# Performance work log

Measured on AMD Instinct MI355X. Metric: run time of the kernel, lower is better.

Reference implementation:

```python
import jax, jax.numpy as jnp
import numpy as np

COMMITMENT_COST = 0.25
DIST_SCALE = 400.0


def setup_inputs() -> dict:
    key = jax.random.key(0)
    ks = jax.random.split(key, 6)
    B, T, D, K = 64, 1024, 512, 512
    s = 1.0 / np.sqrt(D)
    return {
        "inputs": jax.random.normal(ks[0], (B, T, D), dtype=jnp.float32),
        "mean_W": jax.random.normal(ks[1], (D, D), dtype=jnp.float32) * s,
        "mean_b": jax.random.normal(ks[2], (D,), dtype=jnp.float32) * s,
        "logvar_W": jax.random.normal(ks[3], (D, K), dtype=jnp.float32) * s,
        "logvar_b": jax.random.normal(ks[4], (K,), dtype=jnp.float32) * s,
        "embedding": jax.random.normal(ks[5], (K, D), dtype=jnp.float32),
    }


def reference(inputs, mean_W, mean_b, logvar_W, logvar_b, embedding):
    sg = jax.lax.stop_gradient
    D = embedding.shape[1]
    flat = inputs.reshape(-1, D)                      # [N, D]
    x = flat @ mean_W + mean_b                        # mean_layer, [N, D]
    z_logvar = x @ logvar_W + logvar_b                # logvar_layer, [N, K]
    # squared euclidean distances to codebook, [N, K]
    distances = (
        jnp.sum(x * x, axis=1, keepdims=True)
        + jnp.sum(embedding * embedding, axis=1)
        - 2.0 * (x @ embedding.T)
    )
    smooth = jnp.exp(-2.0 * z_logvar)                 # 1/exp(logvar)^2
    d = distances / DIST_SCALE
    prob = jnp.exp(-d * (0.5 * smooth)) / jnp.sqrt(smooth)
    probs = prob / jnp.sum(prob, axis=1, keepdims=True)  # per-row normalize, [N, K]
    quantized = (probs @ embedding).reshape(inputs.shape)
    e_latent_loss = jnp.mean((sg(quantized) - inputs) ** 2)
    q_latent_loss = jnp.mean((quantized - sg(inputs)) ** 2)
    loss = q_latent_loss + COMMITMENT_COST * e_latent_loss
    quantized_st = inputs + sg(quantized - inputs)    # straight-through
    avg_probs = jnp.mean(probs, axis=0)
    perplexity = jnp.exp(-jnp.sum(avg_probs * jnp.log(avg_probs + 1e-10)))
    return loss, quantized_st, perplexity, probs
```

## Files before the change

kernel.cpp:

```cpp
#include <hip/hip_runtime.h>
#include <stdint.h>

#define BM 128
#define BN 128
#define BK 32
#define DIMD 512
#define NROWS 65536
#define QOFF 1
#define PERPOFF 33554433
#define PROBSOFF 33554434
#define NELEM 33554432

typedef __attribute__((ext_vector_type(8))) short bf16x8;
typedef __attribute__((ext_vector_type(4))) short s16x4;
typedef __attribute__((ext_vector_type(4))) float f32x4;

typedef const __attribute__((address_space(1))) void* gas_ptr;
typedef __attribute__((address_space(3))) void* las_ptr;

__device__ __forceinline__ short f2bf(float x){
  uint32_t u = __builtin_bit_cast(uint32_t, x);
  uint32_t r = (u + 0x7fffu + ((u >> 16) & 1u)) >> 16;
  return (short)(uint16_t)r;
}
__device__ __forceinline__ float bf2f(short h){
  return __builtin_bit_cast(float, ((uint32_t)(uint16_t)h) << 16);
}

__device__ __forceinline__ void stage_bf16(const short* __restrict__ g, int row0, int ld, int k0,
                                           short* lds){
  int tid = threadIdx.x;
#pragma unroll
  for (int i = 0; i < 2; ++i){
    int t = tid + i * 256;
    int row = t >> 2, c = t & 3;
    const short* src = g + (long)(row0 + row) * ld + k0 + c * 8;
    __builtin_amdgcn_global_load_lds((gas_ptr)src, (las_ptr)(lds + t * 8), 16, 0, 0);
  }
}

__device__ __forceinline__ void stage_f32_split(const float* __restrict__ g, int row0, int ld, int k0,
                                                short* hi, short* lo){
  int tid = threadIdx.x;
#pragma unroll
  for (int i = 0; i < 4; ++i){
    int t = tid + i * 256;
    int row = t >> 3, c = t & 7;
    const float4 v = *(const float4*)(g + (long)(row0 + row) * ld + k0 + c * 4);
    short h0 = f2bf(v.x), h1 = f2bf(v.y), h2 = f2bf(v.z), h3 = f2bf(v.w);
    s16x4 hv; hv[0] = h0; hv[1] = h1; hv[2] = h2; hv[3] = h3;
    s16x4 lv;
    lv[0] = f2bf(v.x - bf2f(h0)); lv[1] = f2bf(v.y - bf2f(h1));
    lv[2] = f2bf(v.z - bf2f(h2)); lv[3] = f2bf(v.w - bf2f(h3));
    *(s16x4*)(hi + row * BK + c * 4) = hv;
    *(s16x4*)(lo + row * BK + c * 4) = lv;
  }
}

__device__ __forceinline__ bf16x8 frag(const short* lds, int r, int q){
  return *(const bf16x8*)(lds + r * BK + q * 8);
}

__device__ __forceinline__ int swz4(int row, int c){ return c ^ ((row >> 1) & 3); }

__device__ __forceinline__ bf16x8 frag_s(const short* lds, int r, int q){
  return *(const bf16x8*)(lds + r * BK + swz4(r, q) * 8);
}

__device__ __forceinline__ void stage_B512(const short* __restrict__ g, int k0, short* lds){
  int tid = threadIdx.x;
#pragma unroll
  for (int i = 0; i < 4; ++i){
    int t = tid + i * 512;
    int row = t >> 2, c = t & 3;
    int cs = swz4(row, c);
    __builtin_amdgcn_global_load_lds((gas_ptr)(g + (long)row * DIMD + k0 + cs * 8),
                                     (las_ptr)(lds + t * 8), 16, 0, 0);
  }
}

__device__ __forceinline__ void stage_A64(const short* __restrict__ gh, const short* __restrict__ gl,
                                          int n0, int k0, short* Ah, short* Al){
  int tid = threadIdx.x;
  int t = tid & 255;
  int row = t >> 2, c = t & 3;
  int cs = swz4(row, c);
  const short* g = (tid < 256) ? gh : gl;
  short* lds = (tid < 256) ? Ah : Al;
  __builtin_amdgcn_global_load_lds((gas_ptr)(g + (long)(n0 + row) * DIMD + k0 + cs * 8),
                                   (las_ptr)(lds + t * 8), 16, 0, 0);
}

__device__ __forceinline__ void stage_A64h(const short* __restrict__ g, int n0, int k0, short* Ah){
  int tid = threadIdx.x;
  if (tid < 256){
    int row = tid >> 2, c = tid & 3;
    int cs = swz4(row, c);
    __builtin_amdgcn_global_load_lds((gas_ptr)(g + (long)(n0 + row) * DIMD + k0 + cs * 8),
                                     (las_ptr)(Ah + tid * 8), 16, 0, 0);
  }
}

__global__ __launch_bounds__(256) void k_convert_w(
    const float* __restrict__ meanW, const float* __restrict__ lvW, const float* __restrict__ emb,
    short* __restrict__ MWThi, short* __restrict__ MWTlo,
    short* __restrict__ VWThi, short* __restrict__ VWTlo,
    short* __restrict__ E, short* __restrict__ ET, float* __restrict__ enorm)
{
  int b = blockIdx.x;
  int tid = threadIdx.x;
  float esum = 0.f;
  for (int j = tid; j < 512; j += 256){
    float w = meanW[b * 512 + j];
    short h = f2bf(w); short l = f2bf(w - bf2f(h));
    MWThi[j * 512 + b] = h; MWTlo[j * 512 + b] = l;
    float v = lvW[b * 512 + j];
    h = f2bf(v); l = f2bf(v - bf2f(h));
    VWThi[j * 512 + b] = h; VWTlo[j * 512 + b] = l;
    float e = emb[b * 512 + j];
    short eh = f2bf(e);
    E[b * 512 + j] = eh;
    ET[j * 512 + b] = eh;
    esum += e * e;
  }
  for (int o = 32; o >= 1; o >>= 1) esum += __shfl_xor(esum, o);
  __shared__ float red[4];
  if ((tid & 63) == 0) red[tid >> 6] = esum;
  __syncthreads();
  if (tid == 0) enorm[b] = red[0] + red[1] + red[2] + red[3];
}

__global__ __launch_bounds__(256, 2) void k_gemm_mean(
    const float* __restrict__ inp, const short* __restrict__ Bhi, const short* __restrict__ Blo,
    const float* __restrict__ bias, short* __restrict__ Xhi, short* __restrict__ Xlo,
    float* __restrict__ xnorm)
{
  __shared__ short Ah[BM * BK], Al[BM * BK], Bh[BN * BK], Bl[BN * BK];
  int tid = threadIdx.x;
  int n0 = blockIdx.x * BM, c0 = blockIdx.y * BN;
  int lane = tid & 63, wid = tid >> 6;
  int wm = wid >> 1, wn = wid & 1;
  int q = lane >> 4, m = lane & 15;
  f32x4 acc[4][4];
#pragma unroll
  for (int i = 0; i < 4; i++)
#pragma unroll
    for (int j = 0; j < 4; j++)
#pragma unroll
      for (int r = 0; r < 4; r++) acc[i][j][r] = 0.f;

  for (int k0 = 0; k0 < DIMD; k0 += BK){
    __syncthreads();
    stage_f32_split(inp, n0, DIMD, k0, Ah, Al);
    stage_bf16(Bhi, c0, DIMD, k0, Bh);
    stage_bf16(Blo, c0, DIMD, k0, Bl);
    __syncthreads();
    bf16x8 ah[4], al[4], bh[4], bl[4];
#pragma unroll
    for (int i = 0; i < 4; i++){
      ah[i] = frag(Ah, wm * 64 + i * 16 + m, q);
      al[i] = frag(Al, wm * 64 + i * 16 + m, q);
      bh[i] = frag(Bh, wn * 64 + i * 16 + m, q);
      bl[i] = frag(Bl, wn * 64 + i * 16 + m, q);
    }
#pragma unroll
    for (int i = 0; i < 4; i++)
#pragma unroll
      for (int j = 0; j < 4; j++){
        acc[i][j] = __builtin_amdgcn_mfma_f32_16x16x32_bf16(ah[i], bh[j], acc[i][j], 0, 0, 0);
        acc[i][j] = __builtin_amdgcn_mfma_f32_16x16x32_bf16(ah[i], bl[j], acc[i][j], 0, 0, 0);
        acc[i][j] = __builtin_amdgcn_mfma_f32_16x16x32_bf16(al[i], bh[j], acc[i][j], 0, 0, 0);
      }
  }
#pragma unroll
  for (int i = 0; i < 4; i++){
#pragma unroll
    for (int r = 0; r < 4; r++){
      int row = n0 + wm * 64 + i * 16 + q * 4 + r;
      float xn = 0.f;
#pragma unroll
      for (int j = 0; j < 4; j++){
        int col = c0 + wn * 64 + j * 16 + m;
        float x = acc[i][j][r] + bias[col];
        short h = f2bf(x);
        short l = f2bf(x - bf2f(h));
        Xhi[(long)row * DIMD + col] = h;
        Xlo[(long)row * DIMD + col] = l;
        xn += x * x;
      }
      xn += __shfl_xor(xn, 1); xn += __shfl_xor(xn, 2);
      xn += __shfl_xor(xn, 4); xn += __shfl_xor(xn, 8);
      if (m == 0) atomicAdd(&xnorm[row], xn);
    }
  }
}

__global__ __launch_bounds__(512, 2) void k_fused(
    const short* __restrict__ Xh, const short* __restrict__ Xl,
    const short* __restrict__ Vh, const short* __restrict__ Vl,
    const short* __restrict__ Eb, const short* __restrict__ Et,
    const float* __restrict__ lvb, const float* __restrict__ xnorm,
    const float* __restrict__ enorm, const float* __restrict__ inp,
    float* __restrict__ probs, float* __restrict__ qout,
    float* __restrict__ Pacc, float* __restrict__ lossacc)
{
  __shared__ __align__(128) char pool[110592];
  short* Ah  = (short*)pool;
  short* Al  = (short*)(pool + 4096);
  short* Bv0 = (short*)(pool + 8192);
  short* Bv1 = (short*)(pool + 40960);
  short* Be  = (short*)(pool + 73728);
  float* rrA = (float*)(pool + 106496);
  float* rrB = (float*)(pool + 108544);
  short* P   = (short*)(pool + 8192);

  const int tid = threadIdx.x;
  const int n0 = blockIdx.x * 64;
  const int lane = tid & 63, wid = tid >> 6;
  const int q = lane >> 4, m = lane & 15;
  const int c0 = wid * 64;

  f32x4 accZ[4][4];
  f32x4 accS[4][4];
#pragma unroll
  for (int i = 0; i < 4; i++)
#pragma unroll
    for (int j = 0; j < 4; j++)
#pragma unroll
      for (int r = 0; r < 4; r++) accZ[i][j][r] = 0.f;

  stage_A64(Xh, Xl, n0, 0, Ah, Al);
  stage_B512(Vh, 0, Bv0);
  stage_B512(Vl, 0, Bv1);
  for (int k0 = 0; k0 < 512; k0 += 32){
    __syncthreads();
    bf16x8 ah[4], al[4], bh[4], bl[4];
#pragma unroll
    for (int i = 0; i < 4; i++){
      ah[i] = frag_s(Ah, i * 16 + m, q);
      al[i] = frag_s(Al, i * 16 + m, q);
    }
#pragma unroll
    for (int j = 0; j < 4; j++){
      bh[j] = frag_s(Bv0, c0 + j * 16 + m, q);
      bl[j] = frag_s(Bv1, c0 + j * 16 + m, q);
    }
    __syncthreads();
    if (k0 < 480){
      stage_A64(Xh, Xl, n0, k0 + 32, Ah, Al);
      stage_B512(Vh, k0 + 32, Bv0);
      stage_B512(Vl, k0 + 32, Bv1);
    }
#pragma unroll
    for (int j = 0; j < 4; j++)
#pragma unroll
      for (int i = 0; i < 4; i++){
        accZ[i][j] = __builtin_amdgcn_mfma_f32_16x16x32_bf16(ah[i], bh[j], accZ[i][j], 0, 0, 0);
        accZ[i][j] = __builtin_amdgcn_mfma_f32_16x16x32_bf16(ah[i], bl[j], accZ[i][j], 0, 0, 0);
        accZ[i][j] = __builtin_amdgcn_mfma_f32_16x16x32_bf16(al[i], bh[j], accZ[i][j], 0, 0, 0);
      }
  }

#pragma unroll
  for (int i = 0; i < 4; i++)
#pragma unroll
    for (int j = 0; j < 4; j++)
#pragma unroll
      for (int r = 0; r < 4; r++) accS[i][j][r] = 0.f;
  stage_A64h(Xh, n0, 0, Ah);
  stage_B512(Eb, 0, Be);
  for (int k0 = 0; k0 < 512; k0 += 32){
    __syncthreads();
    bf16x8 ah[4], be[4];
#pragma unroll
    for (int i = 0; i < 4; i++) ah[i] = frag_s(Ah, i * 16 + m, q);
#pragma unroll
    for (int j = 0; j < 4; j++) be[j] = frag_s(Be, c0 + j * 16 + m, q);
    __syncthreads();
    if (k0 < 480){
      stage_A64h(Xh, n0, k0 + 32, Ah);
      stage_B512(Eb, k0 + 32, Be);
    }
#pragma unroll
    for (int j = 0; j < 4; j++)
#pragma unroll
      for (int i = 0; i < 4; i++)
        accS[i][j] = __builtin_amdgcn_mfma_f32_16x16x32_bf16(ah[i], be[j], accS[i][j], 0, 0, 0);
  }

  float lvbv[4], env[4];
#pragma unroll
  for (int j = 0; j < 4; j++){
    int col = c0 + j * 16 + m;
    lvbv[j] = lvb[col];
    env[j] = enorm[col];
  }
  float xnv[4][4];
#pragma unroll
  for (int i = 0; i < 4; i++)
#pragma unroll
    for (int r = 0; r < 4; r++) xnv[i][r] = xnorm[n0 + i * 16 + q * 4 + r];

  const float inv800 = 0.5f / 400.0f;
#pragma unroll
  for (int i = 0; i < 4; i++)
#pragma unroll
    for (int j = 0; j < 4; j++)
#pragma unroll
      for (int r = 0; r < 4; r++){
        float z = accZ[i][j][r] + lvbv[j];
        float s = accS[i][j][r];
        float sm = __expf(-2.f * z);
        accS[i][j][r] = z - inv800 * (xnv[i][r] + env[j] - 2.f * s) * sm;
      }

  float mxp[4][4];
#pragma unroll
  for (int i = 0; i < 4; i++)
#pragma unroll
    for (int r = 0; r < 4; r++){
      float v = accS[i][0][r];
#pragma unroll
      for (int j = 1; j < 4; j++) v = fmaxf(v, accS[i][j][r]);
      v = fmaxf(v, __shfl_xor(v, 1));
      v = fmaxf(v, __shfl_xor(v, 2));
      v = fmaxf(v, __shfl_xor(v, 4));
      v = fmaxf(v, __shfl_xor(v, 8));
      mxp[i][r] = v;
    }
  if (m == 0){
#pragma unroll
    for (int i = 0; i < 4; i++)
#pragma unroll
      for (int r = 0; r < 4; r++)
        rrA[(i * 16 + q * 4 + r) * 8 + wid] = mxp[i][r];
  }
  __syncthreads();
  float mxf[4][4];
#pragma unroll
  for (int i = 0; i < 4; i++)
#pragma unroll
    for (int r = 0; r < 4; r++){
      int row = i * 16 + q * 4 + r;
      float v = rrA[row * 8 + 0];
#pragma unroll
      for (int w = 1; w < 8; w++) v = fmaxf(v, rrA[row * 8 + w]);
      mxf[i][r] = v;
    }

  float smr[4][4];
#pragma unroll
  for (int i = 0; i < 4; i++)
#pragma unroll
    for (int r = 0; r < 4; r++){
      float sacc = 0.f;
#pragma unroll
      for (int j = 0; j < 4; j++){
        float p = __expf(accS[i][j][r] - mxf[i][r]);
        accS[i][j][r] = p;
        sacc += p;
      }
      sacc += __shfl_xor(sacc, 1);
      sacc += __shfl_xor(sacc, 2);
      sacc += __shfl_xor(sacc, 4);
      sacc += __shfl_xor(sacc, 8);
      smr[i][r] = sacc;
    }
  if (m == 0){
#pragma unroll
    for (int i = 0; i < 4; i++)
#pragma unroll
      for (int r = 0; r < 4; r++)
        rrB[(i * 16 + q * 4 + r) * 8 + wid] = smr[i][r];
  }
  __syncthreads();
#pragma unroll
  for (int i = 0; i < 4; i++)
#pragma unroll
    for (int r = 0; r < 4; r++){
      int row = i * 16 + q * 4 + r;
      float v = 0.f;
#pragma unroll
      for (int w = 0; w < 8; w++) v += rrB[row * 8 + w];
      smr[i][r] = v;
    }

  float pj[4];
#pragma unroll
  for (int j = 0; j < 4; j++) pj[j] = 0.f;
#pragma unroll
  for (int i = 0; i < 4; i++)
#pragma unroll
    for (int r = 0; r < 4; r++){
      int rowl = i * 16 + q * 4 + r;
      long rowg = n0 + rowl;
      float inv = 1.0f / smr[i][r];
#pragma unroll
      for (int j = 0; j < 4; j++){
        int col = c0 + j * 16 + m;
        float qv = accS[i][j][r] * inv;
        probs[rowg * 512 + col] = qv;
        pj[j] += qv;
        int cg = col >> 3;
        P[rowl * 512 + ((((cg ^ (rowl & 7)) << 3)) | (col & 7))] = f2bf(qv);
      }
    }
#pragma unroll
  for (int j = 0; j < 4; j++){
    pj[j] += __shfl_xor(pj[j], 16);
    pj[j] += __shfl_xor(pj[j], 32);
  }
  if (lane < 16){
#pragma unroll
    for (int j = 0; j < 4; j++) atomicAdd(&Pacc[c0 + j * 16 + m], pj[j]);
  }

#pragma unroll
  for (int i = 0; i < 4; i++)
#pragma unroll
    for (int j = 0; j < 4; j++)
#pragma unroll
      for (int r = 0; r < 4; r++) accZ[i][j][r] = 0.f;
  stage_B512(Et, 0, Be);
  for (int k0 = 0; k0 < 512; k0 += 32){
    __syncthreads();
    bf16x8 pa[4], bq[4];
#pragma unroll
    for (int i = 0; i < 4; i++){
      int rowl = i * 16 + m;
      int cg = (k0 >> 3) + q;
      pa[i] = *(const bf16x8*)(P + rowl * 512 + ((cg ^ (rowl & 7)) << 3));
    }
#pragma unroll
    for (int j = 0; j < 4; j++) bq[j] = frag_s(Be, c0 + j * 16 + m, q);
    __syncthreads();
    if (k0 < 480) stage_B512(Et, k0 + 32, Be);
#pragma unroll
    for (int j = 0; j < 4; j++)
#pragma unroll
      for (int i = 0; i < 4; i++)
        accZ[i][j] = __builtin_amdgcn_mfma_f32_16x16x32_bf16(pa[i], bq[j], accZ[i][j], 0, 0, 0);
  }

  float lsum = 0.f;
#pragma unroll
  for (int i = 0; i < 4; i++)
#pragma unroll
    for (int r = 0; r < 4; r++){
      long rowg = n0 + i * 16 + q * 4 + r;
#pragma unroll
      for (int j = 0; j < 4; j++){
        int col = c0 + j * 16 + m;
        float qv = accZ[i][j][r];
        long idx = rowg * 512 + col;
        qout[idx] = qv;
        float d = qv - inp[idx];
        lsum += d * d;
      }
    }
  lsum += __shfl_xor(lsum, 32);
  lsum += __shfl_xor(lsum, 16);
  lsum += __shfl_xor(lsum, 8);
  lsum += __shfl_xor(lsum, 4);
  lsum += __shfl_xor(lsum, 2);
  lsum += __shfl_xor(lsum, 1);
  if (lane == 0) rrA[wid] = lsum;
  __syncthreads();
  if (tid == 0){
    float t = 0.f;
#pragma unroll
    for (int w = 0; w < 8; w++) t += rrA[w];
    atomicAdd(lossacc, t);
  }
}

__global__ __launch_bounds__(256) void k_final(
    const float* __restrict__ Pacc, const float* __restrict__ lossacc, float* __restrict__ out)
{
  int tid = threadIdx.x;
  float h = 0.f;
  for (int k = tid; k < 512; k += 256){
    float a = Pacc[k] * (1.0f / 65536.0f);
    h += a * __logf(a + 1e-10f);
  }
  for (int o = 32; o >= 1; o >>= 1) h += __shfl_xor(h, o);
  __shared__ float red[4];
  if ((tid & 63) == 0) red[tid >> 6] = h;
  __syncthreads();
  if (tid == 0){
    float H = red[0] + red[1] + red[2] + red[3];
    out[0] = 1.25f * lossacc[0] * (1.0f / (float)NELEM);
    out[PERPOFF] = __expf(-H);
  }
}

extern "C" void kernel_launch(void* const* d_in, const int* in_sizes, int n_in,
                              void* d_out, int out_size, void* d_ws, size_t ws_size,
                              hipStream_t stream)
{
  const float* inp   = (const float*)d_in[0];
  const float* meanW = (const float*)d_in[1];
  const float* meanb = (const float*)d_in[2];
  const float* lvW   = (const float*)d_in[3];
  const float* lvb   = (const float*)d_in[4];
  const float* emb   = (const float*)d_in[5];
  float* out = (float*)d_out;

  char* w = (char*)d_ws;
  short* Xhi = (short*)w;   w += (size_t)NROWS * DIMD * 2;
  short* Xlo = (short*)w;   w += (size_t)NROWS * DIMD * 2;
  short* MWThi = (short*)w; w += 512 * 512 * 2;
  short* MWTlo = (short*)w; w += 512 * 512 * 2;
  short* VWThi = (short*)w; w += 512 * 512 * 2;
  short* VWTlo = (short*)w; w += 512 * 512 * 2;
  short* E     = (short*)w; w += 512 * 512 * 2;
  short* ET    = (short*)w; w += 512 * 512 * 2;
  float* enorm = (float*)w; w += 512 * 4;
  float* stats = (float*)w;
  float* xnorm   = stats;
  float* Pacc    = stats + NROWS;
  float* lossacc = stats + NROWS + 512;

  hipMemsetAsync(stats, 0, (size_t)(NROWS + 512 + 16) * 4, stream);

  k_convert_w<<<512, 256, 0, stream>>>(meanW, lvW, emb, MWThi, MWTlo, VWThi, VWTlo, E, ET, enorm);
  k_gemm_mean<<<dim3(512, 4), 256, 0, stream>>>(inp, MWThi, MWTlo, meanb, Xhi, Xlo, xnorm);
  k_fused<<<1024, 512, 0, stream>>>(Xhi, Xlo, VWThi, VWTlo, E, ET, lvb, xnorm, enorm, inp,
                                    out + PROBSOFF, out + QOFF, Pacc, lossacc);
  k_final<<<1, 256, 0, stream>>>(Pacc, lossacc, out);
}
```

Baseline: 784.4 us.

## Pre-tile operands in global memory and read MFMA fragments directly in fused kernel

Weights, codebook and the bf16 split of the mean-layer output are now written in a k-blocked tiled layout, so the fused kernel loads MFMA fragments straight from global memory instead of staging them through LDS with barriers. The fused kernel moves to 1024 threads (16 waves, 32 columns each), with smaller per-wave accumulators and row reductions done through a compact shared array plus shuffles. This removes LDS staging traffic and most syncthreads, but relies on cache hits for repeated global fragment reads and gives up explicit double buffering and the previous two-blocks-per-CU occupancy.

```diff
diff --git a/kernel.cpp b/kernel.cpp
--- a/kernel.cpp
+++ b/kernel.cpp
@@ -61,50 +61,10 @@
   return *(const bf16x8*)(lds + r * BK + q * 8);
 }
 
-__device__ __forceinline__ int swz4(int row, int c){ return c ^ ((row >> 1) & 3); }
-
-__device__ __forceinline__ bf16x8 frag_s(const short* lds, int r, int q){
-  return *(const bf16x8*)(lds + r * BK + swz4(r, q) * 8);
-}
-
-__device__ __forceinline__ void stage_B512(const short* __restrict__ g, int k0, short* lds){
-  int tid = threadIdx.x;
-#pragma unroll
-  for (int i = 0; i < 4; ++i){
-    int t = tid + i * 512;
-    int row = t >> 2, c = t & 3;
-    int cs = swz4(row, c);
-    __builtin_amdgcn_global_load_lds((gas_ptr)(g + (long)row * DIMD + k0 + cs * 8),
-                                     (las_ptr)(lds + t * 8), 16, 0, 0);
-  }
-}
-
-__device__ __forceinline__ void stage_A64(const short* __restrict__ gh, const short* __restrict__ gl,
-                                          int n0, int k0, short* Ah, short* Al){
-  int tid = threadIdx.x;
-  int t = tid & 255;
-  int row = t >> 2, c = t & 3;
-  int cs = swz4(row, c);
-  const short* g = (tid < 256) ? gh : gl;
-  short* lds = (tid < 256) ? Ah : Al;
-  __builtin_amdgcn_global_load_lds((gas_ptr)(g + (long)(n0 + row) * DIMD + k0 + cs * 8),
-                                   (las_ptr)(lds + t * 8), 16, 0, 0);
-}
-
-__device__ __forceinline__ void stage_A64h(const short* __restrict__ g, int n0, int k0, short* Ah){
-  int tid = threadIdx.x;
-  if (tid < 256){
-    int row = tid >> 2, c = tid & 3;
-    int cs = swz4(row, c);
-    __builtin_amdgcn_global_load_lds((gas_ptr)(g + (long)(n0 + row) * DIMD + k0 + cs * 8),
-                                     (las_ptr)(Ah + tid * 8), 16, 0, 0);
-  }
-}
-
 __global__ __launch_bounds__(256) void k_convert_w(
     const float* __restrict__ meanW, const float* __restrict__ lvW, const float* __restrict__ emb,
     short* __restrict__ MWThi, short* __restrict__ MWTlo,
-    short* __restrict__ VWThi, short* __restrict__ VWTlo,
+    short* __restrict__ VWh, short* __restrict__ VWl,
     short* __restrict__ E, short* __restrict__ ET, float* __restrict__ enorm)
 {
   int b = blockIdx.x;
@@ -116,11 +76,12 @@
     MWThi[j * 512 + b] = h; MWTlo[j * 512 + b] = l;
     float v = lvW[b * 512 + j];
     h = f2bf(v); l = f2bf(v - bf2f(h));
-    VWThi[j * 512 + b] = h; VWTlo[j * 512 + b] = l;
+    long offW = ((long)(b >> 5) << 14) + j * 32 + (b & 31);
+    VWh[offW] = h; VWl[offW] = l;
     float e = emb[b * 512 + j];
     short eh = f2bf(e);
-    E[b * 512 + j] = eh;
-    ET[j * 512 + b] = eh;
+    E[((long)(j >> 5) << 14) + b * 32 + (j & 31)] = eh;
+    ET[((long)(b >> 5) << 14) + j * 32 + (b & 31)] = eh;
     esum += e * e;
   }
   for (int o = 32; o >= 1; o >>= 1) esum += __shfl_xor(esum, o);
@@ -184,8 +145,9 @@
         float x = acc[i][j][r] + bias[col];
         short h = f2bf(x);
         short l = f2bf(x - bf2f(h));
-        Xhi[(long)row * DIMD + col] = h;
-        Xlo[(long)row * DIMD + col] = l;
+        long off = ((long)(row >> 6) << 15) + ((long)(col >> 5) << 11) + (row & 63) * 32 + (col & 31);
+        Xhi[off] = h;
+        Xlo[off] = l;
         xn += x * x;
       }
       xn += __shfl_xor(xn, 1); xn += __shfl_xor(xn, 2);
@@ -195,7 +157,7 @@
   }
 }
 
-__global__ __launch_bounds__(512, 2) void k_fused(
+__global__ __launch_bounds__(1024) void k_fused(
     const short* __restrict__ Xh, const short* __restrict__ Xl,
     const short* __restrict__ Vh, const short* __restrict__ Vl,
     const short* __restrict__ Eb, const short* __restrict__ Et,
@@ -204,55 +166,45 @@
     float* __restrict__ probs, float* __restrict__ qout,
     float* __restrict__ Pacc, float* __restrict__ lossacc)
 {
-  __shared__ __align__(128) char pool[110592];
-  short* Ah  = (short*)pool;
-  short* Al  = (short*)(pool + 4096);
-  short* Bv0 = (short*)(pool + 8192);
-  short* Bv1 = (short*)(pool + 40960);
-  short* Be  = (short*)(pool + 73728);
-  float* rrA = (float*)(pool + 106496);
-  float* rrB = (float*)(pool + 108544);
-  short* P   = (short*)(pool + 8192);
+  __shared__ short P[64 * 512];
+  __shared__ float rrM[16][64];
+  __shared__ float rrS[16][64];
 
   const int tid = threadIdx.x;
   const int n0 = blockIdx.x * 64;
   const int lane = tid & 63, wid = tid >> 6;
   const int q = lane >> 4, m = lane & 15;
-  const int c0 = wid * 64;
-
-  f32x4 accZ[4][4];
-  f32x4 accS[4][4];
-#pragma unroll
-  for (int i = 0; i < 4; i++)
-#pragma unroll
-    for (int j = 0; j < 4; j++)
+  const int c0 = wid * 32;
+
+  const short* Xhb = Xh + (long)blockIdx.x * 32768;
+  const short* Xlb = Xl + (long)blockIdx.x * 32768;
+
+  f32x4 accZ[4][2];
+#pragma unroll
+  for (int i = 0; i < 4; i++)
+#pragma unroll
+    for (int j = 0; j < 2; j++)
 #pragma unroll
       for (int r = 0; r < 4; r++) accZ[i][j][r] = 0.f;
 
-  stage_A64(Xh, Xl, n0, 0, Ah, Al);
-  stage_B512(Vh, 0, Bv0);
-  stage_B512(Vl, 0, Bv1);
-  for (int k0 = 0; k0 < 512; k0 += 32){
-    __syncthreads();
-    bf16x8 ah[4], al[4], bh[4], bl[4];
+  for (int ks = 0; ks < 16; ++ks){
+    const short* xh = Xhb + ks * 2048;
+    const short* xl = Xlb + ks * 2048;
+    const short* vh = Vh + ks * 16384;
+    const short* vl = Vl + ks * 16384;
+    bf16x8 ah[4], al[4], bh[2], bl[2];
 #pragma unroll
     for (int i = 0; i < 4; i++){
-      ah[i] = frag_s(Ah, i * 16 + m, q);
-      al[i] = frag_s(Al, i * 16 + m, q);
-    }
-#pragma unroll
-    for (int j = 0; j < 4; j++){
-      bh[j] = frag_s(Bv0, c0 + j * 16 + m, q);
-      bl[j] = frag_s(Bv1, c0 + j * 16 + m, q);
-    }
-    __syncthreads();
-    if (k0 < 480){
-      stage_A64(Xh, Xl, n0, k0 + 32, Ah, Al);
-      stage_B512(Vh, k0 + 32, Bv0);
-      stage_B512(Vl, k0 + 32, Bv1);
-    }
-#pragma unroll
-    for (int j = 0; j < 4; j++)
+      ah[i] = *(const bf16x8*)(xh + i * 512 + m * 32 + q * 8);
+      al[i] = *(const bf16x8*)(xl + i * 512 + m * 32 + q * 8);
+    }
+#pragma unroll
+    for (int j = 0; j < 2; j++){
+      bh[j] = *(const bf16x8*)(vh + (c0 + j * 16 + m) * 32 + q * 8);
+      bl[j] = *(const bf16x8*)(vl + (c0 + j * 16 + m) * 32 + q * 8);
+    }
+#pragma unroll
+    for (int j = 0; j < 2; j++)
 #pragma unroll
       for (int i = 0; i < 4; i++){
         accZ[i][j] = __builtin_amdgcn_mfma_f32_16x16x32_bf16(ah[i], bh[j], accZ[i][j], 0, 0, 0);
@@ -261,36 +213,31 @@
       }
   }
 
-#pragma unroll
-  for (int i = 0; i < 4; i++)
-#pragma unroll
-    for (int j = 0; j < 4; j++)
+  f32x4 accS[4][2];
+#pragma unroll
+  for (int i = 0; i < 4; i++)
+#pragma unroll
+    for (int j = 0; j < 2; j++)
 #pragma unroll
       for (int r = 0; r < 4; r++) accS[i][j][r] = 0.f;
-  stage_A64h(Xh, n0, 0, Ah);
-  stage_B512(Eb, 0, Be);
-  for (int k0 = 0; k0 < 512; k0 += 32){
-    __syncthreads();
-    bf16x8 ah[4], be[4];
-#pragma unroll
-    for (int i = 0; i < 4; i++) ah[i] = frag_s(Ah, i * 16 + m, q);
-#pragma unroll
-    for (int j = 0; j < 4; j++) be[j] = frag_s(Be, c0 + j * 16 + m, q);
-    __syncthreads();
-    if (k0 < 480){
-      stage_A64h(Xh, n0, k0 + 32, Ah);
-      stage_B512(Eb, k0 + 32, Be);
-    }
-#pragma unroll
-    for (int j = 0; j < 4; j++)
+  for (int ks = 0; ks < 16; ++ks){
+    const short* xh = Xhb + ks * 2048;
+    const short* eb = Eb + ks * 16384;
+    bf16x8 ah[4], be[2];
+#pragma unroll
+    for (int i = 0; i < 4; i++) ah[i] = *(const bf16x8*)(xh + i * 512 + m * 32 + q * 8);
+#pragma unroll
+    for (int j = 0; j < 2; j++) be[j] = *(const bf16x8*)(eb + (c0 + j * 16 + m) * 32 + q * 8);
+#pragma unroll
+    for (int j = 0; j < 2; j++)
 #pragma unroll
       for (int i = 0; i < 4; i++)
         accS[i][j] = __builtin_amdgcn_mfma_f32_16x16x32_bf16(ah[i], be[j], accS[i][j], 0, 0, 0);
   }
 
-  float lvbv[4], env[4];
-#pragma unroll
-  for (int j = 0; j < 4; j++){
+  float lvbv[2], env[2];
+#pragma unroll
+  for (int j = 0; j < 2; j++){
     int col = c0 + j * 16 + m;
     lvbv[j] = lvb[col];
     env[j] = enorm[col];
@@ -305,7 +252,7 @@
 #pragma unroll
   for (int i = 0; i < 4; i++)
 #pragma unroll
-    for (int j = 0; j < 4; j++)
+    for (int j = 0; j < 2; j++)
 #pragma unroll
       for (int r = 0; r < 4; r++){
         float z = accZ[i][j][r] + lvbv[j];
@@ -314,48 +261,38 @@
         accS[i][j][r] = z - inv800 * (xnv[i][r] + env[j] - 2.f * s) * sm;
       }
 
-  float mxp[4][4];
 #pragma unroll
   for (int i = 0; i < 4; i++)
 #pragma unroll
     for (int r = 0; r < 4; r++){
-      float v = accS[i][0][r];
-#pragma unroll
-      for (int j = 1; j < 4; j++) v = fmaxf(v, accS[i][j][r]);
+      float v = fmaxf(accS[i][0][r], accS[i][1][r]);
       v = fmaxf(v, __shfl_xor(v, 1));
       v = fmaxf(v, __shfl_xor(v, 2));
       v = fmaxf(v, __shfl_xor(v, 4));
       v = fmaxf(v, __shfl_xor(v, 8));
-      mxp[i][r] = v;
-    }
-  if (m == 0){
-#pragma unroll
-    for (int i = 0; i < 4; i++)
-#pragma unroll
-      for (int r = 0; r < 4; r++)
-        rrA[(i * 16 + q * 4 + r) * 8 + wid] = mxp[i][r];
-  }
-  __syncthreads();
+      if (m == 0) rrM[wid][i * 16 + q * 4 + r] = v;
+    }
+  __syncthreads();
+  float rmax;
+  {
+    float v = rrM[0][lane];
+#pragma unroll
+    for (int w = 1; w < 16; w++) v = fmaxf(v, rrM[w][lane]);
+    rmax = v;
+  }
   float mxf[4][4];
 #pragma unroll
   for (int i = 0; i < 4; i++)
 #pragma unroll
-    for (int r = 0; r < 4; r++){
-      int row = i * 16 + q * 4 + r;
-      float v = rrA[row * 8 + 0];
-#pragma unroll
-      for (int w = 1; w < 8; w++) v = fmaxf(v, rrA[row * 8 + w]);
-      mxf[i][r] = v;
-    }
-
-  float smr[4][4];
+    for (int r = 0; r < 4; r++) mxf[i][r] = __shfl(rmax, i * 16 + q * 4 + r);
+
 #pragma unroll
   for (int i = 0; i < 4; i++)
 #pragma unroll
     for (int r = 0; r < 4; r++){
       float sacc = 0.f;
 #pragma unroll
-      for (int j = 0; j < 4; j++){
+      for (int j = 0; j < 2; j++){
         float p = __expf(accS[i][j][r] - mxf[i][r]);
         accS[i][j][r] = p;
         sacc += p;
@@ -364,30 +301,24 @@
       sacc += __shfl_xor(sacc, 2);
       sacc += __shfl_xor(sacc, 4);
       sacc += __shfl_xor(sacc, 8);
-      smr[i][r] = sacc;
-    }
-  if (m == 0){
-#pragma unroll
-    for (int i = 0; i < 4; i++)
-#pragma unroll
-      for (int r = 0; r < 4; r++)
-        rrB[(i * 16 + q * 4 + r) * 8 + wid] = smr[i][r];
-  }
-  __syncthreads();
-#pragma unroll
-  for (int i = 0; i < 4; i++)
-#pragma unroll
-    for (int r = 0; r < 4; r++){
-      int row = i * 16 + q * 4 + r;
-      float v = 0.f;
-#pragma unroll
-      for (int w = 0; w < 8; w++) v += rrB[row * 8 + w];
-      smr[i][r] = v;
-    }
-
-  float pj[4];
-#pragma unroll
-  for (int j = 0; j < 4; j++) pj[j] = 0.f;
+      if (m == 0) rrS[wid][i * 16 + q * 4 + r] = sacc;
+    }
+  __syncthreads();
+  float rsum;
+  {
+    float v = 0.f;
+#pragma unroll
+    for (int w = 0; w < 16; w++) v += rrS[w][lane];
+    rsum = v;
+  }
+  float smr[4][4];
+#pragma unroll
+  for (int i = 0; i < 4; i++)
+#pragma unroll
+    for (int r = 0; r < 4; r++) smr[i][r] = __shfl(rsum, i * 16 + q * 4 + r);
+
+  float pj[2];
+  pj[0] = 0.f; pj[1] = 0.f;
 #pragma unroll
   for (int i = 0; i < 4; i++)
 #pragma unroll
@@ -396,35 +327,37 @@
       long rowg = n0 + rowl;
       float inv = 1.0f / smr[i][r];
 #pragma unroll
-      for (int j = 0; j < 4; j++){
+      for (int j = 0; j < 2; j++){
         int col = c0 + j * 16 + m;
         float qv = accS[i][j][r] * inv;
         probs[rowg * 512 + col] = qv;
         pj[j] += qv;
         int cg = col >> 3;
-        P[rowl * 512 + ((((cg ^ (rowl & 7)) << 3)) | (col & 7))] = f2bf(qv);
-      }
-    }
-#pragma unroll
-  for (int j = 0; j < 4; j++){
+        P[rowl * 512 + (((cg ^ (rowl & 7)) << 3) | (col & 7))] = f2bf(qv);
+      }
+    }
+#pragma unroll
+  for (int j = 0; j < 2; j++){
     pj[j] += __shfl_xor(pj[j], 16);
     pj[j] += __shfl_xor(pj[j], 32);
   }
   if (lane < 16){
 #pragma unroll
-    for (int j = 0; j < 4; j++) atomicAdd(&Pacc[c0 + j * 16 + m], pj[j]);
-  }
-
-#pragma unroll
-  for (int i = 0; i < 4; i++)
-#pragma unroll
-    for (int j = 0; j < 4; j++)
-#pragma unroll
-      for (int r = 0; r < 4; r++) accZ[i][j][r] = 0.f;
-  stage_B512(Et, 0, Be);
-  for (int k0 = 0; k0 < 512; k0 += 32){
-    __syncthreads();
-    bf16x8 pa[4], bq[4];
+    for (int j = 0; j < 2; j++) atomicAdd(&Pacc[c0 + j * 16 + m], pj[j]);
+  }
+  __syncthreads();
+
+  f32x4 accQ[4][2];
+#pragma unroll
+  for (int i = 0; i < 4; i++)
+#pragma unroll
+    for (int j = 0; j < 2; j++)
+#pragma unroll
+      for (int r = 0; r < 4; r++) accQ[i][j][r] = 0.f;
+  for (int ks = 0; ks < 16; ++ks){
+    int k0 = ks * 32;
+    const short* et = Et + ks * 16384;
+    bf16x8 pa[4], bq[2];
 #pragma unroll
     for (int i = 0; i < 4; i++){
       int rowl = i * 16 + m;
@@ -432,14 +365,12 @@
       pa[i] = *(const bf16x8*)(P + rowl * 512 + ((cg ^ (rowl & 7)) << 3));
     }
 #pragma unroll
-    for (int j = 0; j < 4; j++) bq[j] = frag_s(Be, c0 + j * 16 + m, q);
-    __syncthreads();
-    if (k0 < 480) stage_B512(Et, k0 + 32, Be);
-#pragma unroll
-    for (int j = 0; j < 4; j++)
+    for (int j = 0; j < 2; j++) bq[j] = *(const bf16x8*)(et + (c0 + j * 16 + m) * 32 + q * 8);
+#pragma unroll
+    for (int j = 0; j < 2; j++)
 #pragma unroll
       for (int i = 0; i < 4; i++)
-        accZ[i][j] = __builtin_amdgcn_mfma_f32_16x16x32_bf16(pa[i], bq[j], accZ[i][j], 0, 0, 0);
+        accQ[i][j] = __builtin_amdgcn_mfma_f32_16x16x32_bf16(pa[i], bq[j], accQ[i][j], 0, 0, 0);
   }
 
   float lsum = 0.f;
@@ -449,9 +380,9 @@
     for (int r = 0; r < 4; r++){
       long rowg = n0 + i * 16 + q * 4 + r;
 #pragma unroll
-      for (int j = 0; j < 4; j++){
+      for (int j = 0; j < 2; j++){
         int col = c0 + j * 16 + m;
-        float qv = accZ[i][j][r];
+        float qv = accQ[i][j][r];
         long idx = rowg * 512 + col;
         qout[idx] = qv;
         float d = qv - inp[idx];
@@ -464,12 +395,12 @@
   lsum += __shfl_xor(lsum, 4);
   lsum += __shfl_xor(lsum, 2);
   lsum += __shfl_xor(lsum, 1);
-  if (lane == 0) rrA[wid] = lsum;
+  if (lane == 0) rrM[0][wid] = lsum;
   __syncthreads();
   if (tid == 0){
     float t = 0.f;
 #pragma unroll
-    for (int w = 0; w < 8; w++) t += rrA[w];
+    for (int w = 0; w < 16; w++) t += rrM[0][w];
     atomicAdd(lossacc, t);
   }
 }
@@ -511,8 +442,8 @@
   short* Xlo = (short*)w;   w += (size_t)NROWS * DIMD * 2;
   short* MWThi = (short*)w; w += 512 * 512 * 2;
   short* MWTlo = (short*)w; w += 512 * 512 * 2;
-  short* VWThi = (short*)w; w += 512 * 512 * 2;
-  short* VWTlo = (short*)w; w += 512 * 512 * 2;
+  short* VWh   = (short*)w; w += 512 * 512 * 2;
+  short* VWl   = (short*)w; w += 512 * 512 * 2;
   short* E     = (short*)w; w += 512 * 512 * 2;
   short* ET    = (short*)w; w += 512 * 512 * 2;
   float* enorm = (float*)w; w += 512 * 4;
@@ -523,9 +454,9 @@
 
   hipMemsetAsync(stats, 0, (size_t)(NROWS + 512 + 16) * 4, stream);
 
-  k_convert_w<<<512, 256, 0, stream>>>(meanW, lvW, emb, MWThi, MWTlo, VWThi, VWTlo, E, ET, enorm);
+  k_convert_w<<<512, 256, 0, stream>>>(meanW, lvW, emb, MWThi, MWTlo, VWh, VWl, E, ET, enorm);
   k_gemm_mean<<<dim3(512, 4), 256, 0, stream>>>(inp, MWThi, MWTlo, meanb, Xhi, Xlo, xnorm);
-  k_fused<<<1024, 512, 0, stream>>>(Xhi, Xlo, VWThi, VWTlo, E, ET, lvb, xnorm, enorm, inp,
-                                    out + PROBSOFF, out + QOFF, Pacc, lossacc);
+  k_fused<<<1024, 1024, 0, stream>>>(Xhi, Xlo, VWh, VWl, E, ET, lvb, xnorm, enorm, inp,
+                                     out + PROBSOFF, out + QOFF, Pacc, lossacc);
   k_final<<<1, 256, 0, stream>>>(Pacc, lossacc, out);
 }
```

After: 870.4 us. 11.0% more time.
